# Optimization experiments

Hardware: AMD Instinct MI355X
Metric: run time of the kernel (lower is better)

The kernel has to match this reference:

```python
import jax, jax.numpy as jnp
import numpy as np

N = 50000      # num_nodes
E = 800000     # num_edges
D = 128        # hidden_dim
V = 32000      # vocab_size
T = 8          # num_edge_types
NT = 16        # num_node_types


def setup_inputs() -> dict:
    key = jax.random.key(0)
    ks = jax.random.split(key, 10)
    s = 1.0 / np.sqrt(D)
    return {
        "x": jax.random.randint(ks[0], (N,), 0, V),
        "edge_index": jax.random.randint(ks[1], (2, E), 0, N),
        "edge_type": jax.random.randint(ks[2], (E,), 0, T),
        "node_type": jax.random.randint(ks[3], (N,), 0, NT),
        "emb": jax.random.normal(ks[4], (V, D), dtype=jnp.float32) * s,
        "W_rel": jax.random.normal(ks[5], (T, D, D), dtype=jnp.float32) * s,
        "b_node": jax.random.normal(ks[6], (NT, D), dtype=jnp.float32) * 0.01,
        "W_ih": jax.random.normal(ks[7], (3 * D, D), dtype=jnp.float32) * s,
        "W_hh": jax.random.normal(ks[8], (3 * D, D), dtype=jnp.float32) * s,
        "b_ih": jnp.zeros((3 * D,), dtype=jnp.float32),
        "b_hh": jnp.zeros((3 * D,), dtype=jnp.float32),
    }


def _gru_cell(inp, h, W_ih, W_hh, b_ih, b_hh):
    # torch.nn.GRUCell semantics
    gi = inp @ W_ih.T + b_ih   # [N, 3D]
    gh = h @ W_hh.T + b_hh     # [N, 3D]
    i_r, i_z, i_n = jnp.split(gi, 3, axis=-1)
    h_r, h_z, h_n = jnp.split(gh, 3, axis=-1)
    r = jax.nn.sigmoid(i_r + h_r)
    z = jax.nn.sigmoid(i_z + h_z)
    n = jnp.tanh(i_n + r * h_n)
    return (1.0 - z) * n + z * h


def reference(x, edge_index, edge_type, node_type, emb, W_rel, b_node, W_ih, W_hh, b_ih, b_hh):
    h = emb[x]                                   # [N, D] node embeddings
    src, dst = edge_index[0], edge_index[1]
    n_nodes = h.shape[0]
    for _ in range(5):
        # relational message passing: per-edge-type linear on source nodes
        Ht = jnp.einsum('nd,tdf->ntf', h, W_rel)  # [N, T, D] all-type transforms
        msg = Ht[src, edge_type]                  # [E, D] gather per edge
        aggr = jax.ops.segment_sum(msg, dst, num_segments=n_nodes)  # scatter-add to dst
        aggr = aggr + b_node[node_type]           # node-type-specific bias
        h = _gru_cell(aggr, h, W_ih, W_hh, b_ih, b_hh)
    return h
```

## Files before the change

kernel.cpp:

```cpp
#include <hip/hip_runtime.h>
#include <hip/hip_fp16.h>
#include <math.h>

#define N_NODES 50000
#define N_EDGES 800000
#define D 128
#define T_TYPES 8
#define TPAD 136
#define NBLK_SCAN 196
#define TILES 1563
#define GRID_GRU 256

typedef short short8 __attribute__((ext_vector_type(8)));
typedef unsigned short ushort4v __attribute__((ext_vector_type(4)));
typedef float float4v __attribute__((ext_vector_type(4)));
typedef unsigned short ushort_t;

static __device__ __forceinline__ unsigned short f2bf(float f) {
    unsigned u = __float_as_uint(f);
    u += 0x7fff + ((u >> 16) & 1);
    return (unsigned short)(u >> 16);
}
static __device__ __forceinline__ float bf2f(unsigned short b) {
    return __uint_as_float((unsigned)b << 16);
}
static __device__ __forceinline__ void splitbf(float x, unsigned short& hi, unsigned short& lo) {
    unsigned short h_ = f2bf(x);
    hi = h_;
    lo = f2bf(x - bf2f(h_));
}

#define GLOAD16(gp, lp) __builtin_amdgcn_global_load_lds( \
    (const __attribute__((address_space(1))) unsigned int*)(gp), \
    (__attribute__((address_space(3))) unsigned int*)(lp), 16, 0, 0)

__global__ void embed_gather(const int* __restrict__ x, const float* __restrict__ emb,
                             ushort_t* __restrict__ hhi, ushort_t* __restrict__ hlo) {
    int n = blockIdx.x;
    int d = threadIdx.x;
    float v = emb[(size_t)x[n] * D + d];
    unsigned short a, b;
    splitbf(v, a, b);
    hhi[(size_t)n * D + d] = a;
    hlo[(size_t)n * D + d] = b;
}

__global__ void convert_wrelT(const float* __restrict__ Wrel,
                              ushort_t* __restrict__ hi, ushort_t* __restrict__ lo) {
    int idx = blockIdx.x * 256 + threadIdx.x;
    int t = idx >> 14;
    int rem = idx & 16383;
    int f = rem >> 7;
    int d = rem & 127;
    unsigned short a, b;
    splitbf(Wrel[((size_t)t << 14) + (d << 7) + f], a, b);
    hi[idx] = a;
    lo[idx] = b;
}

__global__ void convert_w(const float* __restrict__ in,
                          ushort_t* __restrict__ hi, ushort_t* __restrict__ lo, int n) {
    int idx = blockIdx.x * 256 + threadIdx.x;
    if (idx < n) {
        unsigned short a, b;
        splitbf(in[idx], a, b);
        hi[idx] = a;
        lo[idx] = b;
    }
}

__global__ void count_deg(const int* __restrict__ ei, int* __restrict__ deg) {
    int e = blockIdx.x * 256 + threadIdx.x;
    if (e >= N_EDGES) return;
    atomicAdd(&deg[ei[N_EDGES + e]], 1);
}

__global__ __launch_bounds__(256) void scan_blocks(const int* __restrict__ deg,
                                                   int* __restrict__ bsums) {
    __shared__ int red[4];
    int idx = blockIdx.x * 256 + threadIdx.x;
    int v = (idx < N_NODES) ? deg[idx] : 0;
#pragma unroll
    for (int o = 32; o > 0; o >>= 1) v += __shfl_down(v, o);
    if ((threadIdx.x & 63) == 0) red[threadIdx.x >> 6] = v;
    __syncthreads();
    if (threadIdx.x == 0) bsums[blockIdx.x] = red[0] + red[1] + red[2] + red[3];
}

__global__ __launch_bounds__(256) void scan_tops(int* __restrict__ bsums) {
    __shared__ int s[256];
    int tid = threadIdx.x;
    int v = (tid < NBLK_SCAN) ? bsums[tid] : 0;
    s[tid] = v;
    __syncthreads();
#pragma unroll
    for (int o = 1; o < 256; o <<= 1) {
        int u = (tid >= o) ? s[tid - o] : 0;
        __syncthreads();
        s[tid] += u;
        __syncthreads();
    }
    if (tid < NBLK_SCAN) bsums[tid] = s[tid] - v;
}

__global__ __launch_bounds__(256) void scan_final(const int* __restrict__ bsums,
                                                  int* __restrict__ deg_cursor,
                                                  int* __restrict__ rs) {
    __shared__ int s[256];
    int tid = threadIdx.x;
    int idx = blockIdx.x * 256 + tid;
    int v = (idx < N_NODES) ? deg_cursor[idx] : 0;
    s[tid] = v;
    __syncthreads();
#pragma unroll
    for (int o = 1; o < 256; o <<= 1) {
        int u = (tid >= o) ? s[tid - o] : 0;
        __syncthreads();
        s[tid] += u;
        __syncthreads();
    }
    int excl = s[tid] - v + bsums[blockIdx.x];
    if (idx < N_NODES) {
        rs[idx] = excl;
        deg_cursor[idx] = excl;
    }
    if (idx == 0) rs[N_NODES] = N_EDGES;
}

__global__ void fill_csr(const int* __restrict__ ei, const int* __restrict__ et,
                         int* __restrict__ cursor, int* __restrict__ packed) {
    int e = blockIdx.x * 256 + threadIdx.x;
    if (e >= N_EDGES) return;
    int dst = ei[N_EDGES + e];
    int pos = atomicAdd(&cursor[dst], 1);
    packed[pos] = (ei[e] << 3) | et[e];
}

__global__ __launch_bounds__(256, 2) void gemm_rel(const ushort_t* __restrict__ hhi,
                                                   const ushort_t* __restrict__ hlo,
                                                   const ushort_t* __restrict__ Whi,
                                                   const ushort_t* __restrict__ Wlo,
                                                   ushort_t* __restrict__ Ht) {
    __shared__ __align__(16) ushort_t wlds[2][128 * TPAD];
    const int tid = threadIdx.x;
    const int wave = tid >> 6, lane = tid & 63;
    const int q = lane >> 4, li = lane & 15;
    const int t = blockIdx.y;
    const int m_base = blockIdx.x * 128 + wave * 32;

    {
        const ushort_t* gh = Whi + ((size_t)t << 14);
        const ushort_t* gl = Wlo + ((size_t)t << 14);
#pragma unroll
        for (int i = 0; i < 8; ++i) {
            int g = (i * 256 + tid) * 8;
            int row = g >> 7, col = g & 127;
            *(short8*)(&wlds[0][row * TPAD + col]) = *(const short8*)(gh + g);
            *(short8*)(&wlds[1][row * TPAD + col]) = *(const short8*)(gl + g);
        }
    }
    __syncthreads();

    int r0 = m_base + li;      if (r0 > N_NODES - 1) r0 = N_NODES - 1;
    int r1 = m_base + 16 + li; if (r1 > N_NODES - 1) r1 = N_NODES - 1;
    const ushort_t* A0h = hhi + (size_t)r0 * D + q * 8;
    const ushort_t* A0l = hlo + (size_t)r0 * D + q * 8;
    const ushort_t* A1h = hhi + (size_t)r1 * D + q * 8;
    const ushort_t* A1l = hlo + (size_t)r1 * D + q * 8;

    short8 a0h[4], a0l[4], a1h[4], a1l[4];
#pragma unroll
    for (int ks = 0; ks < 4; ++ks) {
        a0h[ks] = *(const short8*)(A0h + ks * 32);
        a0l[ks] = *(const short8*)(A0l + ks * 32);
        a1h[ks] = *(const short8*)(A1h + ks * 32);
        a1l[ks] = *(const short8*)(A1l + ks * 32);
    }

    float4v acc[2][8];
#pragma unroll
    for (int m = 0; m < 2; ++m)
#pragma unroll
        for (int ft = 0; ft < 8; ++ft) acc[m][ft] = (float4v){0.f, 0.f, 0.f, 0.f};

#pragma unroll
    for (int ks = 0; ks < 4; ++ks) {
#pragma unroll
        for (int ft = 0; ft < 8; ++ft) {
            const int lo_off = (ft * 16 + li) * TPAD + ks * 32 + q * 8;
            short8 bh = *(const short8*)(&wlds[0][lo_off]);
            short8 bl = *(const short8*)(&wlds[1][lo_off]);
            acc[0][ft] = __builtin_amdgcn_mfma_f32_16x16x32_bf16(a0h[ks], bh, acc[0][ft], 0, 0, 0);
            acc[0][ft] = __builtin_amdgcn_mfma_f32_16x16x32_bf16(a0l[ks], bh, acc[0][ft], 0, 0, 0);
            acc[0][ft] = __builtin_amdgcn_mfma_f32_16x16x32_bf16(a0h[ks], bl, acc[0][ft], 0, 0, 0);
            acc[1][ft] = __builtin_amdgcn_mfma_f32_16x16x32_bf16(a1h[ks], bh, acc[1][ft], 0, 0, 0);
            acc[1][ft] = __builtin_amdgcn_mfma_f32_16x16x32_bf16(a1l[ks], bh, acc[1][ft], 0, 0, 0);
            acc[1][ft] = __builtin_amdgcn_mfma_f32_16x16x32_bf16(a1h[ks], bl, acc[1][ft], 0, 0, 0);
        }
    }

    __syncthreads();
    ushort_t* tw = &wlds[0][0] + wave * 32 * TPAD;
#pragma unroll
    for (int m = 0; m < 2; ++m)
#pragma unroll
        for (int ft = 0; ft < 8; ++ft)
#pragma unroll
            for (int r = 0; r < 4; ++r) {
                __half hv = __float2half_rn(acc[m][ft][r]);
                tw[(m * 16 + q * 4 + r) * TPAD + ft * 16 + li] = __half_as_ushort(hv);
            }
#pragma unroll
    for (int i = 0; i < 8; ++i) {
        int row = i * 4 + q;
        int col = li * 8;
        short8 v = *(const short8*)(tw + row * TPAD + col);
        int orow = m_base + row;
        if (orow < N_NODES)
            *(short8*)(Ht + (size_t)orow * 1024 + (t << 7) + col) = v;
    }
}

__global__ __launch_bounds__(256) void aggregate_csr(const int* __restrict__ rs,
                                                     const int* __restrict__ packed,
                                                     const ushort_t* __restrict__ Ht,
                                                     const int* __restrict__ nt,
                                                     const float* __restrict__ b_node,
                                                     ushort_t* __restrict__ ahi,
                                                     ushort_t* __restrict__ alo) {
    int n = blockIdx.x * 4 + (threadIdx.x >> 6);
    if (n >= N_NODES) return;
    const int lane = threadIdx.x & 63;
    const int beg = rs[n], end = rs[n + 1];
    const __half2* Ht2 = (const __half2*)Ht;

    float2 acc = ((const float2*)(b_node + (size_t)nt[n] * D))[lane];

    int i = beg;
    for (; i + 3 < end; i += 4) {
        int p0 = packed[i], p1 = packed[i + 1], p2 = packed[i + 2], p3 = packed[i + 3];
        float2 f0 = __half22float2(Ht2[(size_t)p0 * 64 + lane]);
        float2 f1 = __half22float2(Ht2[(size_t)p1 * 64 + lane]);
        float2 f2 = __half22float2(Ht2[(size_t)p2 * 64 + lane]);
        float2 f3 = __half22float2(Ht2[(size_t)p3 * 64 + lane]);
        acc.x += (f0.x + f1.x) + (f2.x + f3.x);
        acc.y += (f0.y + f1.y) + (f2.y + f3.y);
    }
    for (; i < end; ++i) {
        int pk = packed[i];
        float2 fv = __half22float2(Ht2[(size_t)pk * 64 + lane]);
        acc.x += fv.x;
        acc.y += fv.y;
    }

    unsigned short h0, l0, h1, l1;
    splitbf(acc.x, h0, l0);
    splitbf(acc.y, h1, l1);
    ((unsigned*)ahi)[(size_t)n * 64 + lane] = (unsigned)h0 | ((unsigned)h1 << 16);
    ((unsigned*)alo)[(size_t)n * 64 + lane] = (unsigned)l0 | ((unsigned)l1 << 16);
}

__global__ __launch_bounds__(512, 2) void gru_persist(
    const ushort_t* __restrict__ ahi, const ushort_t* __restrict__ alo,
    const ushort_t* __restrict__ hhi_in, const ushort_t* __restrict__ hlo_in,
    ushort_t* __restrict__ hhi_out, ushort_t* __restrict__ hlo_out,
    const ushort_t* __restrict__ Wihi, const ushort_t* __restrict__ Wilo,
    const ushort_t* __restrict__ Whhi, const ushort_t* __restrict__ Whlo,
    const float* __restrict__ b_ih, const float* __restrict__ b_hh,
    float* __restrict__ h, int write_h)
{
    __shared__ __align__(16) ushort_t xlds[2][4][4096];

    const int tid = threadIdx.x;
    const int w = tid >> 6, lane = tid & 63;
    const int q = lane >> 4, li = lane & 15;
    const int fg = w * 16 + li;
    const int f0 = w * 16 + q * 4;

    const size_t oR = (size_t)fg * D + q * 8;
    const size_t oZ = (size_t)(D + fg) * D + q * 8;
    const size_t oN = (size_t)(2 * D + fg) * D + q * 8;
    short8 Wr[12][4];
#pragma unroll
    for (int ks = 0; ks < 4; ++ks) {
        const int off = ks * 32;
        Wr[0][ks]  = *(const short8*)(Wihi + oR + off);
        Wr[1][ks]  = *(const short8*)(Wilo + oR + off);
        Wr[2][ks]  = *(const short8*)(Whhi + oR + off);
        Wr[3][ks]  = *(const short8*)(Whlo + oR + off);
        Wr[4][ks]  = *(const short8*)(Wihi + oZ + off);
        Wr[5][ks]  = *(const short8*)(Wilo + oZ + off);
        Wr[6][ks]  = *(const short8*)(Whhi + oZ + off);
        Wr[7][ks]  = *(const short8*)(Whlo + oZ + off);
        Wr[8][ks]  = *(const short8*)(Wihi + oN + off);
        Wr[9][ks]  = *(const short8*)(Wilo + oN + off);
        Wr[10][ks] = *(const short8*)(Whhi + oN + off);
        Wr[11][ks] = *(const short8*)(Whlo + oN + off);
    }
    float4v bR4 = *(const float4v*)(b_ih + f0);
    float4v bZ4 = *(const float4v*)(b_ih + D + f0);
    float4v bIn4 = *(const float4v*)(b_ih + 2 * D + f0);
    {
        float4v t0 = *(const float4v*)(b_hh + f0);
        float4v t1 = *(const float4v*)(b_hh + D + f0);
        bR4 += t0; bZ4 += t1;
    }
    float4v bHn4 = *(const float4v*)(b_hh + 2 * D + f0);

    const int lrow = w * 4 + (lane >> 4);
    const int cswz = (lane & 15) ^ (lrow & 7);

#define STAGE(BUF_, TILE_) do {                                      \
        int gr_ = (TILE_) * 32 + lrow;                               \
        if (gr_ > N_NODES - 1) gr_ = N_NODES - 1;                    \
        const size_t so_ = (size_t)gr_ * D + cswz * 8;               \
        ushort_t* lb_ = &xlds[BUF_][0][0] + (w * 4) * 128;           \
        GLOAD16(ahi + so_,    lb_);                                  \
        GLOAD16(alo + so_,    lb_ + 4096);                           \
        GLOAD16(hhi_in + so_, lb_ + 8192);                           \
        GLOAD16(hlo_in + so_, lb_ + 12288);                          \
    } while (0)

    const int s = blockIdx.x;
    STAGE(0, s);
    __syncthreads();

    int cur = 0;
    for (int tile = s; tile < TILES; tile += GRID_GRU) {
        const int nxt = tile + GRID_GRU;
        if (nxt < TILES) STAGE(cur ^ 1, nxt);

        const ushort_t* xb = &xlds[cur][0][0];
        float4v aR[2], aZ[2], aI[2], aH[2];
#pragma unroll
        for (int m = 0; m < 2; ++m) {
            aR[m] = (float4v){0.f, 0.f, 0.f, 0.f};
            aZ[m] = aR[m]; aI[m] = aR[m]; aH[m] = aR[m];
        }
#pragma unroll
        for (int ks = 0; ks < 4; ++ks) {
#pragma unroll
            for (int m = 0; m < 2; ++m) {
                const int row = m * 16 + li;
                const int inoff = row * 128 + ((ks * 32 + q * 8) ^ ((row & 7) << 3));
                short8 xah = *(const short8*)(xb + inoff);
                short8 xal = *(const short8*)(xb + 4096 + inoff);
                short8 xhh = *(const short8*)(xb + 8192 + inoff);
                short8 xhl = *(const short8*)(xb + 12288 + inoff);
                aR[m] = __builtin_amdgcn_mfma_f32_16x16x32_bf16(Wr[0][ks], xah, aR[m], 0, 0, 0);
                aR[m] = __builtin_amdgcn_mfma_f32_16x16x32_bf16(Wr[0][ks], xal, aR[m], 0, 0, 0);
                aR[m] = __builtin_amdgcn_mfma_f32_16x16x32_bf16(Wr[1][ks], xah, aR[m], 0, 0, 0);
                aR[m] = __builtin_amdgcn_mfma_f32_16x16x32_bf16(Wr[2][ks], xhh, aR[m], 0, 0, 0);
                aR[m] = __builtin_amdgcn_mfma_f32_16x16x32_bf16(Wr[2][ks], xhl, aR[m], 0, 0, 0);
                aR[m] = __builtin_amdgcn_mfma_f32_16x16x32_bf16(Wr[3][ks], xhh, aR[m], 0, 0, 0);
                aZ[m] = __builtin_amdgcn_mfma_f32_16x16x32_bf16(Wr[4][ks], xah, aZ[m], 0, 0, 0);
                aZ[m] = __builtin_amdgcn_mfma_f32_16x16x32_bf16(Wr[4][ks], xal, aZ[m], 0, 0, 0);
                aZ[m] = __builtin_amdgcn_mfma_f32_16x16x32_bf16(Wr[5][ks], xah, aZ[m], 0, 0, 0);
                aZ[m] = __builtin_amdgcn_mfma_f32_16x16x32_bf16(Wr[6][ks], xhh, aZ[m], 0, 0, 0);
                aZ[m] = __builtin_amdgcn_mfma_f32_16x16x32_bf16(Wr[6][ks], xhl, aZ[m], 0, 0, 0);
                aZ[m] = __builtin_amdgcn_mfma_f32_16x16x32_bf16(Wr[7][ks], xhh, aZ[m], 0, 0, 0);
                aI[m] = __builtin_amdgcn_mfma_f32_16x16x32_bf16(Wr[8][ks], xah, aI[m], 0, 0, 0);
                aI[m] = __builtin_amdgcn_mfma_f32_16x16x32_bf16(Wr[8][ks], xal, aI[m], 0, 0, 0);
                aI[m] = __builtin_amdgcn_mfma_f32_16x16x32_bf16(Wr[9][ks], xah, aI[m], 0, 0, 0);
                aH[m] = __builtin_amdgcn_mfma_f32_16x16x32_bf16(Wr[10][ks], xhh, aH[m], 0, 0, 0);
                aH[m] = __builtin_amdgcn_mfma_f32_16x16x32_bf16(Wr[10][ks], xhl, aH[m], 0, 0, 0);
                aH[m] = __builtin_amdgcn_mfma_f32_16x16x32_bf16(Wr[11][ks], xhh, aH[m], 0, 0, 0);
            }
        }

#pragma unroll
        for (int m = 0; m < 2; ++m) {
            const int node = tile * 32 + m * 16 + li;
            const int row = m * 16 + li;
            const int chunk = (f0 >> 3) ^ (row & 7);
            const int hoff = row * 128 + chunk * 8 + (q & 1) * 4;
            ushort4v hh4 = *(const ushort4v*)(xb + 8192 + hoff);
            ushort4v hl4 = *(const ushort4v*)(xb + 12288 + hoff);
            if (node < N_NODES) {
                ushort4v sh4, sl4;
                float4v hn4;
#pragma unroll
                for (int r = 0; r < 4; ++r) {
                    float hold = bf2f(hh4[r]) + bf2f(hl4[r]);
                    float rg = 1.0f / (1.0f + __expf(-(aR[m][r] + bR4[r])));
                    float zg = 1.0f / (1.0f + __expf(-(aZ[m][r] + bZ4[r])));
                    float narg = aI[m][r] + bIn4[r] + rg * (aH[m][r] + bHn4[r]);
                    float ex = __expf(2.0f * narg);
                    float ng = 1.0f - 2.0f / (ex + 1.0f);
                    float hn = (1.0f - zg) * ng + zg * hold;
                    hn4[r] = hn;
                    unsigned short sh, sl;
                    splitbf(hn, sh, sl);
                    sh4[r] = sh;
                    sl4[r] = sl;
                }
                const size_t go = (size_t)node * D + f0;
                *(ushort4v*)(hhi_out + go) = sh4;
                *(ushort4v*)(hlo_out + go) = sl4;
                if (write_h) *(float4v*)(h + go) = hn4;
            }
        }
        __syncthreads();
        cur ^= 1;
    }
#undef STAGE
}

extern "C" void kernel_launch(void* const* d_in, const int* in_sizes, int n_in,
                              void* d_out, int out_size, void* d_ws, size_t ws_size,
                              hipStream_t stream) {
    const int* x      = (const int*)d_in[0];
    const int* ei     = (const int*)d_in[1];
    const int* et     = (const int*)d_in[2];
    const int* nt     = (const int*)d_in[3];
    const float* emb  = (const float*)d_in[4];
    const float* Wrel = (const float*)d_in[5];
    const float* b_node = (const float*)d_in[6];
    const float* W_ih = (const float*)d_in[7];
    const float* W_hh = (const float*)d_in[8];
    const float* b_ih = (const float*)d_in[9];
    const float* b_hh = (const float*)d_in[10];

    float* h = (float*)d_out;
    float* ws = (float*)d_ws;

    ushort_t* Ht = (ushort_t*)ws;
    ushort_t* us = (ushort_t*)(ws + 25600000);
    ushort_t* ahi  = us;
    ushort_t* alo  = us + 6400000;
    ushort_t* hhi  = us + 12800000;
    ushort_t* hlo  = us + 19200000;
    ushort_t* Whi  = us + 25600000;
    ushort_t* Wlo  = Whi + 131072;
    ushort_t* Wihi = Wlo + 131072;
    ushort_t* Wilo = Wihi + 49152;
    ushort_t* Whhi = Wilo + 49152;
    ushort_t* Whlo = Whhi + 49152;
    int* rs     = (int*)(ws + 38629376);
    int* packed = rs + 50004;
    int* bsums  = packed + 800000;
    ushort_t* hhi2 = (ushort_t*)(ws + 39479808);
    ushort_t* hlo2 = hhi2 + 6400000;
    int* deg    = (int*)ws;

    convert_wrelT<<<512, 256, 0, stream>>>(Wrel, Whi, Wlo);
    convert_w<<<192, 256, 0, stream>>>(W_ih, Wihi, Wilo, 3 * D * D);
    convert_w<<<192, 256, 0, stream>>>(W_hh, Whhi, Whlo, 3 * D * D);
    embed_gather<<<N_NODES, 128, 0, stream>>>(x, emb, hhi, hlo);

    hipMemsetAsync(deg, 0, 50000 * sizeof(int), stream);
    count_deg<<<3125, 256, 0, stream>>>(ei, deg);
    scan_blocks<<<NBLK_SCAN, 256, 0, stream>>>(deg, bsums);
    scan_tops<<<1, 256, 0, stream>>>(bsums);
    scan_final<<<NBLK_SCAN, 256, 0, stream>>>(bsums, deg, rs);
    fill_csr<<<3125, 256, 0, stream>>>(ei, et, deg, packed);

    for (int it = 0; it < 5; ++it) {
        const ushort_t* hi_in = (it & 1) ? hhi2 : hhi;
        const ushort_t* lo_in = (it & 1) ? hlo2 : hlo;
        ushort_t* hi_out = (it & 1) ? hhi : hhi2;
        ushort_t* lo_out = (it & 1) ? hlo : hlo2;
        dim3 g(391, T_TYPES);
        gemm_rel<<<g, 256, 0, stream>>>(hi_in, lo_in, Whi, Wlo, Ht);
        aggregate_csr<<<12500, 256, 0, stream>>>(rs, packed, Ht, nt, b_node, ahi, alo);
        gru_persist<<<GRID_GRU, 512, 0, stream>>>(ahi, alo, hi_in, lo_in, hi_out, lo_out,
                                                  Wihi, Wilo, Whhi, Whlo, b_ih, b_hh,
                                                  h, it == 4 ? 1 : 0);
    }
}
```

Baseline: 999.4 us.

## Fuse relational per-type GEMM into GRU kernel epilogue for next iteration

The GRU kernel now computes the next iteration's per-edge-type transform Ht directly from the freshly produced hidden state, staged through LDS. This removes the separate gemm_rel launch and its reread of h for iterations 1-4, with only the initial Ht computed up front. GRU weights are no longer kept resident in registers but reloaded per k-step from global/L2, to free registers for higher occupancy (launch bounds 4, grid doubled to 512). The trade-off is more global weight traffic and a longer per-tile epilogue, and the GRU epilogue now runs for out-of-range rows too.

```diff
diff --git a/kernel.cpp b/kernel.cpp
--- a/kernel.cpp
+++ b/kernel.cpp
@@ -9,7 +9,7 @@
 #define TPAD 136
 #define NBLK_SCAN 196
 #define TILES 1563
-#define GRID_GRU 256
+#define GRID_GRU 512
 
 typedef short short8 __attribute__((ext_vector_type(8)));
 typedef unsigned short ushort4v __attribute__((ext_vector_type(4)));
@@ -260,16 +260,19 @@
     ((unsigned*)alo)[(size_t)n * 64 + lane] = (unsigned)l0 | ((unsigned)l1 << 16);
 }
 
-__global__ __launch_bounds__(512, 2) void gru_persist(
+__global__ __launch_bounds__(512, 4) void gru_gemm_fused(
     const ushort_t* __restrict__ ahi, const ushort_t* __restrict__ alo,
     const ushort_t* __restrict__ hhi_in, const ushort_t* __restrict__ hlo_in,
     ushort_t* __restrict__ hhi_out, ushort_t* __restrict__ hlo_out,
     const ushort_t* __restrict__ Wihi, const ushort_t* __restrict__ Wilo,
     const ushort_t* __restrict__ Whhi, const ushort_t* __restrict__ Whlo,
+    const ushort_t* __restrict__ Whi, const ushort_t* __restrict__ Wlo,
     const float* __restrict__ b_ih, const float* __restrict__ b_hh,
-    float* __restrict__ h, int write_h)
+    float* __restrict__ h, ushort_t* __restrict__ Ht,
+    int write_ht, int write_h)
 {
     __shared__ __align__(16) ushort_t xlds[2][4][4096];
+    __shared__ __align__(16) ushort_t hbuf[2][4096];
 
     const int tid = threadIdx.x;
     const int w = tid >> 6, lane = tid & 63;
@@ -277,26 +280,10 @@
     const int fg = w * 16 + li;
     const int f0 = w * 16 + q * 4;
 
-    const size_t oR = (size_t)fg * D + q * 8;
-    const size_t oZ = (size_t)(D + fg) * D + q * 8;
-    const size_t oN = (size_t)(2 * D + fg) * D + q * 8;
-    short8 Wr[12][4];
-#pragma unroll
-    for (int ks = 0; ks < 4; ++ks) {
-        const int off = ks * 32;
-        Wr[0][ks]  = *(const short8*)(Wihi + oR + off);
-        Wr[1][ks]  = *(const short8*)(Wilo + oR + off);
-        Wr[2][ks]  = *(const short8*)(Whhi + oR + off);
-        Wr[3][ks]  = *(const short8*)(Whlo + oR + off);
-        Wr[4][ks]  = *(const short8*)(Wihi + oZ + off);
-        Wr[5][ks]  = *(const short8*)(Wilo + oZ + off);
-        Wr[6][ks]  = *(const short8*)(Whhi + oZ + off);
-        Wr[7][ks]  = *(const short8*)(Whlo + oZ + off);
-        Wr[8][ks]  = *(const short8*)(Wihi + oN + off);
-        Wr[9][ks]  = *(const short8*)(Wilo + oN + off);
-        Wr[10][ks] = *(const short8*)(Whhi + oN + off);
-        Wr[11][ks] = *(const short8*)(Whlo + oN + off);
-    }
+    const size_t oR = (size_t)fg * D;
+    const size_t oZ = (size_t)(D + fg) * D;
+    const size_t oN = (size_t)(2 * D + fg) * D;
+
     float4v bR4 = *(const float4v*)(b_ih + f0);
     float4v bZ4 = *(const float4v*)(b_ih + D + f0);
     float4v bIn4 = *(const float4v*)(b_ih + 2 * D + f0);
@@ -322,6 +309,7 @@
     } while (0)
 
     const int s = blockIdx.x;
+    if (s * 32 >= N_NODES + 31) return;
     STAGE(0, s);
     __syncthreads();
 
@@ -339,6 +327,19 @@
         }
 #pragma unroll
         for (int ks = 0; ks < 4; ++ks) {
+            const size_t wo = (size_t)(ks * 32 + q * 8);
+            short8 wIRh = *(const short8*)(Wihi + oR + wo);
+            short8 wIRl = *(const short8*)(Wilo + oR + wo);
+            short8 wHRh = *(const short8*)(Whhi + oR + wo);
+            short8 wHRl = *(const short8*)(Whlo + oR + wo);
+            short8 wIZh = *(const short8*)(Wihi + oZ + wo);
+            short8 wIZl = *(const short8*)(Wilo + oZ + wo);
+            short8 wHZh = *(const short8*)(Whhi + oZ + wo);
+            short8 wHZl = *(const short8*)(Whlo + oZ + wo);
+            short8 wINh = *(const short8*)(Wihi + oN + wo);
+            short8 wINl = *(const short8*)(Wilo + oN + wo);
+            short8 wHNh = *(const short8*)(Whhi + oN + wo);
+            short8 wHNl = *(const short8*)(Whlo + oN + wo);
 #pragma unroll
             for (int m = 0; m < 2; ++m) {
                 const int row = m * 16 + li;
@@ -347,24 +348,24 @@
                 short8 xal = *(const short8*)(xb + 4096 + inoff);
                 short8 xhh = *(const short8*)(xb + 8192 + inoff);
                 short8 xhl = *(const short8*)(xb + 12288 + inoff);
-                aR[m] = __builtin_amdgcn_mfma_f32_16x16x32_bf16(Wr[0][ks], xah, aR[m], 0, 0, 0);
-                aR[m] = __builtin_amdgcn_mfma_f32_16x16x32_bf16(Wr[0][ks], xal, aR[m], 0, 0, 0);
-                aR[m] = __builtin_amdgcn_mfma_f32_16x16x32_bf16(Wr[1][ks], xah, aR[m], 0, 0, 0);
-                aR[m] = __builtin_amdgcn_mfma_f32_16x16x32_bf16(Wr[2][ks], xhh, aR[m], 0, 0, 0);
-                aR[m] = __builtin_amdgcn_mfma_f32_16x16x32_bf16(Wr[2][ks], xhl, aR[m], 0, 0, 0);
-                aR[m] = __builtin_amdgcn_mfma_f32_16x16x32_bf16(Wr[3][ks], xhh, aR[m], 0, 0, 0);
-                aZ[m] = __builtin_amdgcn_mfma_f32_16x16x32_bf16(Wr[4][ks], xah, aZ[m], 0, 0, 0);
-                aZ[m] = __builtin_amdgcn_mfma_f32_16x16x32_bf16(Wr[4][ks], xal, aZ[m], 0, 0, 0);
-                aZ[m] = __builtin_amdgcn_mfma_f32_16x16x32_bf16(Wr[5][ks], xah, aZ[m], 0, 0, 0);
-                aZ[m] = __builtin_amdgcn_mfma_f32_16x16x32_bf16(Wr[6][ks], xhh, aZ[m], 0, 0, 0);
-                aZ[m] = __builtin_amdgcn_mfma_f32_16x16x32_bf16(Wr[6][ks], xhl, aZ[m], 0, 0, 0);
-                aZ[m] = __builtin_amdgcn_mfma_f32_16x16x32_bf16(Wr[7][ks], xhh, aZ[m], 0, 0, 0);
-                aI[m] = __builtin_amdgcn_mfma_f32_16x16x32_bf16(Wr[8][ks], xah, aI[m], 0, 0, 0);
-                aI[m] = __builtin_amdgcn_mfma_f32_16x16x32_bf16(Wr[8][ks], xal, aI[m], 0, 0, 0);
-                aI[m] = __builtin_amdgcn_mfma_f32_16x16x32_bf16(Wr[9][ks], xah, aI[m], 0, 0, 0);
-                aH[m] = __builtin_amdgcn_mfma_f32_16x16x32_bf16(Wr[10][ks], xhh, aH[m], 0, 0, 0);
-                aH[m] = __builtin_amdgcn_mfma_f32_16x16x32_bf16(Wr[10][ks], xhl, aH[m], 0, 0, 0);
-                aH[m] = __builtin_amdgcn_mfma_f32_16x16x32_bf16(Wr[11][ks], xhh, aH[m], 0, 0, 0);
+                aR[m] = __builtin_amdgcn_mfma_f32_16x16x32_bf16(wIRh, xah, aR[m], 0, 0, 0);
+                aR[m] = __builtin_amdgcn_mfma_f32_16x16x32_bf16(wIRh, xal, aR[m], 0, 0, 0);
+                aR[m] = __builtin_amdgcn_mfma_f32_16x16x32_bf16(wIRl, xah, aR[m], 0, 0, 0);
+                aR[m] = __builtin_amdgcn_mfma_f32_16x16x32_bf16(wHRh, xhh, aR[m], 0, 0, 0);
+                aR[m] = __builtin_amdgcn_mfma_f32_16x16x32_bf16(wHRh, xhl, aR[m], 0, 0, 0);
+                aR[m] = __builtin_amdgcn_mfma_f32_16x16x32_bf16(wHRl, xhh, aR[m], 0, 0, 0);
+                aZ[m] = __builtin_amdgcn_mfma_f32_16x16x32_bf16(wIZh, xah, aZ[m], 0, 0, 0);
+                aZ[m] = __builtin_amdgcn_mfma_f32_16x16x32_bf16(wIZh, xal, aZ[m], 0, 0, 0);
+                aZ[m] = __builtin_amdgcn_mfma_f32_16x16x32_bf16(wIZl, xah, aZ[m], 0, 0, 0);
+                aZ[m] = __builtin_amdgcn_mfma_f32_16x16x32_bf16(wHZh, xhh, aZ[m], 0, 0, 0);
+                aZ[m] = __builtin_amdgcn_mfma_f32_16x16x32_bf16(wHZh, xhl, aZ[m], 0, 0, 0);
+                aZ[m] = __builtin_amdgcn_mfma_f32_16x16x32_bf16(wHZl, xhh, aZ[m], 0, 0, 0);
+                aI[m] = __builtin_amdgcn_mfma_f32_16x16x32_bf16(wINh, xah, aI[m], 0, 0, 0);
+                aI[m] = __builtin_amdgcn_mfma_f32_16x16x32_bf16(wINh, xal, aI[m], 0, 0, 0);
+                aI[m] = __builtin_amdgcn_mfma_f32_16x16x32_bf16(wINl, xah, aI[m], 0, 0, 0);
+                aH[m] = __builtin_amdgcn_mfma_f32_16x16x32_bf16(wHNh, xhh, aH[m], 0, 0, 0);
+                aH[m] = __builtin_amdgcn_mfma_f32_16x16x32_bf16(wHNh, xhl, aH[m], 0, 0, 0);
+                aH[m] = __builtin_amdgcn_mfma_f32_16x16x32_bf16(wHNl, xhh, aH[m], 0, 0, 0);
             }
         }
 
@@ -376,28 +377,79 @@
             const int hoff = row * 128 + chunk * 8 + (q & 1) * 4;
             ushort4v hh4 = *(const ushort4v*)(xb + 8192 + hoff);
             ushort4v hl4 = *(const ushort4v*)(xb + 12288 + hoff);
+            ushort4v sh4, sl4;
+            float4v hn4;
+#pragma unroll
+            for (int r = 0; r < 4; ++r) {
+                float hold = bf2f(hh4[r]) + bf2f(hl4[r]);
+                float rg = 1.0f / (1.0f + __expf(-(aR[m][r] + bR4[r])));
+                float zg = 1.0f / (1.0f + __expf(-(aZ[m][r] + bZ4[r])));
+                float narg = aI[m][r] + bIn4[r] + rg * (aH[m][r] + bHn4[r]);
+                float ex = __expf(2.0f * narg);
+                float ng = 1.0f - 2.0f / (ex + 1.0f);
+                float hn = (1.0f - zg) * ng + zg * hold;
+                hn4[r] = hn;
+                unsigned short sh, sl;
+                splitbf(hn, sh, sl);
+                sh4[r] = sh;
+                sl4[r] = sl;
+            }
             if (node < N_NODES) {
-                ushort4v sh4, sl4;
-                float4v hn4;
-#pragma unroll
-                for (int r = 0; r < 4; ++r) {
-                    float hold = bf2f(hh4[r]) + bf2f(hl4[r]);
-                    float rg = 1.0f / (1.0f + __expf(-(aR[m][r] + bR4[r])));
-                    float zg = 1.0f / (1.0f + __expf(-(aZ[m][r] + bZ4[r])));
-                    float narg = aI[m][r] + bIn4[r] + rg * (aH[m][r] + bHn4[r]);
-                    float ex = __expf(2.0f * narg);
-                    float ng = 1.0f - 2.0f / (ex + 1.0f);
-                    float hn = (1.0f - zg) * ng + zg * hold;
-                    hn4[r] = hn;
-                    unsigned short sh, sl;
-                    splitbf(hn, sh, sl);
-                    sh4[r] = sh;
-                    sl4[r] = sl;
-                }
                 const size_t go = (size_t)node * D + f0;
                 *(ushort4v*)(hhi_out + go) = sh4;
                 *(ushort4v*)(hlo_out + go) = sl4;
                 if (write_h) *(float4v*)(h + go) = hn4;
+            }
+            if (write_ht) {
+                *(ushort4v*)(&hbuf[0][hoff]) = sh4;
+                *(ushort4v*)(&hbuf[1][hoff]) = sl4;
+            }
+        }
+
+        if (write_ht) {
+            __syncthreads();
+            float4v hacc[8][2];
+#pragma unroll
+            for (int ft = 0; ft < 8; ++ft) {
+                hacc[ft][0] = (float4v){0.f, 0.f, 0.f, 0.f};
+                hacc[ft][1] = hacc[ft][0];
+            }
+#pragma unroll
+            for (int ks = 0; ks < 4; ++ks) {
+                short8 bhh[2], bhl[2];
+#pragma unroll
+                for (int m = 0; m < 2; ++m) {
+                    const int row = m * 16 + li;
+                    const int off = row * 128 + (((ks * 4 + q) ^ (row & 7)) << 3);
+                    bhh[m] = *(const short8*)(&hbuf[0][off]);
+                    bhl[m] = *(const short8*)(&hbuf[1][off]);
+                }
+#pragma unroll
+                for (int ft = 0; ft < 8; ++ft) {
+                    const size_t wo = ((size_t)w << 14) + (ft * 16 + li) * 128 + ks * 32 + q * 8;
+                    short8 aWh = *(const short8*)(Whi + wo);
+                    short8 aWl = *(const short8*)(Wlo + wo);
+                    hacc[ft][0] = __builtin_amdgcn_mfma_f32_16x16x32_bf16(aWh, bhh[0], hacc[ft][0], 0, 0, 0);
+                    hacc[ft][0] = __builtin_amdgcn_mfma_f32_16x16x32_bf16(aWh, bhl[0], hacc[ft][0], 0, 0, 0);
+                    hacc[ft][0] = __builtin_amdgcn_mfma_f32_16x16x32_bf16(aWl, bhh[0], hacc[ft][0], 0, 0, 0);
+                    hacc[ft][1] = __builtin_amdgcn_mfma_f32_16x16x32_bf16(aWh, bhh[1], hacc[ft][1], 0, 0, 0);
+                    hacc[ft][1] = __builtin_amdgcn_mfma_f32_16x16x32_bf16(aWh, bhl[1], hacc[ft][1], 0, 0, 0);
+                    hacc[ft][1] = __builtin_amdgcn_mfma_f32_16x16x32_bf16(aWl, bhh[1], hacc[ft][1], 0, 0, 0);
+                }
+            }
+#pragma unroll
+            for (int ft = 0; ft < 8; ++ft) {
+#pragma unroll
+                for (int m = 0; m < 2; ++m) {
+                    const int node = tile * 32 + m * 16 + li;
+                    if (node < N_NODES) {
+                        ushort4v o;
+#pragma unroll
+                        for (int r = 0; r < 4; ++r)
+                            o[r] = __half_as_ushort(__float2half_rn(hacc[ft][m][r]));
+                        *(ushort4v*)(Ht + (size_t)node * 1024 + (w << 7) + ft * 16 + q * 4) = o;
+                    }
+                }
             }
         }
         __syncthreads();
@@ -455,16 +507,20 @@
     scan_final<<<NBLK_SCAN, 256, 0, stream>>>(bsums, deg, rs);
     fill_csr<<<3125, 256, 0, stream>>>(ei, et, deg, packed);
 
+    {
+        dim3 g(391, T_TYPES);
+        gemm_rel<<<g, 256, 0, stream>>>(hhi, hlo, Whi, Wlo, Ht);
+    }
+
     for (int it = 0; it < 5; ++it) {
         const ushort_t* hi_in = (it & 1) ? hhi2 : hhi;
         const ushort_t* lo_in = (it & 1) ? hlo2 : hlo;
         ushort_t* hi_out = (it & 1) ? hhi : hhi2;
         ushort_t* lo_out = (it & 1) ? hlo : hlo2;
-        dim3 g(391, T_TYPES);
-        gemm_rel<<<g, 256, 0, stream>>>(hi_in, lo_in, Whi, Wlo, Ht);
         aggregate_csr<<<12500, 256, 0, stream>>>(rs, packed, Ht, nt, b_node, ahi, alo);
-        gru_persist<<<GRID_GRU, 512, 0, stream>>>(ahi, alo, hi_in, lo_in, hi_out, lo_out,
-                                                  Wihi, Wilo, Whhi, Whlo, b_ih, b_hh,
-                                                  h, it == 4 ? 1 : 0);
-    }
-}
+        gru_gemm_fused<<<GRID_GRU, 512, 0, stream>>>(
+            ahi, alo, hi_in, lo_in, hi_out, lo_out,
+            Wihi, Wilo, Whhi, Whlo, Whi, Wlo, b_ih, b_hh,
+            h, Ht, it < 4 ? 1 : 0, it == 4 ? 1 : 0);
+    }
+}
```

Result: slower. 2.694 ms (+169.6%).
